# Kernel tuning notes

Measured on AMD Instinct MI355X. Metric: run time of the kernel, lower is better.

The kernel has to match this reference:

```python
import jax, jax.numpy as jnp
import numpy as np

NH, NKV, HD = 16, 8, 128  # heads, kv heads, head dim
N_REP = NH // NKV
EPS = 1e-06
K_MASK = float(jnp.finfo(jnp.bfloat16).min)
SCALE = HD ** -0.5


def _rms_norm(x, w):
    xf = x.astype(jnp.float32)
    rms = jnp.sqrt(jnp.mean(xf * xf, axis=-1, keepdims=True) + EPS)
    return (xf / rms * w).astype(x.dtype)


def _rotate_half(x):
    x1, x2 = jnp.split(x, 2, axis=-1)
    return jnp.concatenate([-x2, x1], axis=-1)


def setup_inputs() -> dict:
    key = jax.random.key(0)
    ks = jax.random.split(key, 5)
    B, S, H = 1, 2048, 2048
    hidden_states = jax.random.normal(ks[0], (B, S, H), jnp.float32)
    # real RoPE tables (duplicated-half layout), theta = 5e6
    pos = jnp.arange(S, dtype=jnp.float32)
    inv_freq = 1.0 / (5_000_000.0 ** (jnp.arange(0, HD, 2, dtype=jnp.float32) / HD))
    ang = pos[:, None] * inv_freq[None, :]            # (S, HD/2)
    emb = jnp.concatenate([ang, ang], axis=-1)[None]  # (1, S, HD)
    cos, sin = jnp.cos(emb), jnp.sin(emb)
    attention_mask = jnp.tril(jnp.ones((S, S), bool))[None, None]  # causal (1,1,S,S)
    sc = 0.02
    wq = jax.random.normal(ks[1], (H, NH * HD), jnp.float32) * sc
    wk = jax.random.normal(ks[2], (H, NKV * HD), jnp.float32) * sc
    wv = jax.random.normal(ks[3], (H, NKV * HD), jnp.float32) * sc
    wo = jax.random.normal(ks[4], (NH * HD, H), jnp.float32) * sc
    q_norm_w = jnp.ones((HD,), jnp.float32)
    k_norm_w = jnp.ones((HD,), jnp.float32)
    return {"hidden_states": hidden_states, "cos": cos, "sin": sin,
            "attention_mask": attention_mask, "wq": wq, "wk": wk, "wv": wv,
            "wo": wo, "q_norm_w": q_norm_w, "k_norm_w": k_norm_w}


def reference(hidden_states, cos, sin, attention_mask, wq, wk, wv, wo, q_norm_w, k_norm_w):
    B, S, H = hidden_states.shape
    q = (hidden_states @ wq).reshape(B, S, NH, HD)
    k = (hidden_states @ wk).reshape(B, S, NKV, HD)
    v = (hidden_states @ wv).reshape(B, S, NKV, HD)
    q = _rms_norm(q, q_norm_w)
    k = _rms_norm(k, k_norm_w)
    c = cos[:, :, None, :]
    s = sin[:, :, None, :]
    q = q * c + _rotate_half(q) * s
    k = k * c + _rotate_half(k) * s
    # GQA: group q heads by kv head; same math as jnp.repeat + matmul
    qg = q.reshape(B, S, NKV, N_REP, HD)
    scores = jnp.einsum('bqgrd,bkgd->bgrqk', qg, k) * SCALE  # (B,NKV,N_REP,S,S)
    scores = jnp.where(attention_mask[:, :, None], scores, K_MASK)
    attn = jax.nn.softmax(scores.astype(jnp.float32), axis=-1).astype(q.dtype)
    out = jnp.einsum('bgrqk,bkgd->bqgrd', attn, v)            # (B,S,NKV,N_REP,HD)
    out = out.reshape(B, S, NH * HD)
    return out @ wo
```

## Files before the change

kernel.cpp:

```cpp
#include <hip/hip_runtime.h>
#include <hip/hip_bf16.h>
#include <stdint.h>

typedef _Float16 half8 __attribute__((ext_vector_type(8)));
typedef _Float16 half4 __attribute__((ext_vector_type(4)));
typedef float f32x4 __attribute__((ext_vector_type(4)));

#define MFMA16(A, B, C) __builtin_amdgcn_mfma_f32_16x16x32_f16(A, B, C, 0, 0, 0)

static constexpr int Sdim = 2048;
static constexpr int NH = 16;
static constexpr int NKV = 8;
static constexpr int HD = 128;
static constexpr float ATT_SCALE = 0.08838834764831845f;
static constexpr float S0 = 4.0f;

__device__ __forceinline__ void async_copy16(const _Float16* g, _Float16* l) {
  auto gp = reinterpret_cast<const __attribute__((address_space(1))) uint32_t*>(
      reinterpret_cast<uintptr_t>(g));
  auto lp = reinterpret_cast<__attribute__((address_space(3))) uint32_t*>(
      reinterpret_cast<uintptr_t>(l));
  __builtin_amdgcn_global_load_lds(gp, lp, 16, 0, 0);
}

__global__ __launch_bounds__(256) void xconv(const float* __restrict__ X,
                                             _Float16* __restrict__ Xh) {
  int i = (blockIdx.x * 256 + threadIdx.x) * 4;
  float4 v = *(const float4*)(X + i);
  half4 h = {(_Float16)v.x, (_Float16)v.y, (_Float16)v.z, (_Float16)v.w};
  *(half4*)(Xh + i) = h;
}

__global__ __launch_bounds__(256) void wtrans_all(const float* __restrict__ wq,
                                                  const float* __restrict__ wk,
                                                  const float* __restrict__ wv,
                                                  const float* __restrict__ wo,
                                                  _Float16* __restrict__ wqT,
                                                  _Float16* __restrict__ wkT,
                                                  _Float16* __restrict__ wvT,
                                                  _Float16* __restrict__ woT) {
  const float* W;
  _Float16* WT;
  int N;
  switch (blockIdx.z) {
    case 0: W = wq; WT = wqT; N = 2048; break;
    case 1: W = wk; WT = wkT; N = 1024; break;
    case 2: W = wv; WT = wvT; N = 1024; break;
    default: W = wo; WT = woT; N = 2048; break;
  }
  if ((int)blockIdx.x * 64 >= N) return;
  const int K = 2048;
  __shared__ __align__(16) float tile[64][68];
  int n0 = blockIdx.x * 64, k0 = blockIdx.y * 64;
  int t = threadIdx.x;
  int c = (t & 15) * 4;
  int rb = t >> 4;
  for (int p = 0; p < 4; ++p) {
    int k = p * 16 + rb;
    *(float4*)&tile[k][c] = *(const float4*)(W + (size_t)(k0 + k) * N + n0 + c);
  }
  __syncthreads();
  int n = t >> 2;
  int kc = (t & 3) * 16;
  half8 o0, o1;
  for (int i = 0; i < 8; ++i) {
    o0[i] = (_Float16)tile[kc + i][n];
    o1[i] = (_Float16)tile[kc + 8 + i][n];
  }
  _Float16* dst = WT + (size_t)(n0 + n) * K + k0 + kc;
  *(half8*)dst = o0;
  *(half8*)(dst + 8) = o1;
}

template <int NI>
__device__ __forceinline__ void stage64(const _Float16* __restrict__ src, size_t stride,
                                        int k0, _Float16* lds, int w, int lane) {
  for (int ii = 0; ii < NI; ++ii) {
    int i = w * NI + ii;
    int row = i * 8 + (lane >> 3);
    int c = (lane & 7) ^ (row & 7);
    async_copy16(src + (size_t)row * stride + k0 + c * 8, lds + i * 512);
  }
}

__device__ __forceinline__ int frag_off(int row, int ks, int quad, int col) {
  return row * 64 + (((ks << 2) | quad) ^ (col & 7)) * 8;
}

__global__ __launch_bounds__(256) void gemm_qkv(const _Float16* __restrict__ Xh,
                                                const _Float16* __restrict__ wqT,
                                                const _Float16* __restrict__ wkT,
                                                const _Float16* __restrict__ wvT,
                                                _Float16* __restrict__ Q,
                                                _Float16* __restrict__ K,
                                                _Float16* __restrict__ Vt) {
  __shared__ __align__(16) _Float16 As[128 * 64];
  __shared__ __align__(16) _Float16 Bs[128 * 64];
  int bx = blockIdx.x, m0 = blockIdx.y * 128;
  const _Float16* BT;
  _Float16* outp;
  int n0, Nst;
  bool vt;
  if (bx < 16)      { BT = wqT; outp = Q;  n0 = bx * 128;        vt = false; Nst = 2048; }
  else if (bx < 24) { BT = wkT; outp = K;  n0 = (bx - 16) * 128; vt = false; Nst = 1024; }
  else              { BT = wvT; outp = Vt; n0 = (bx - 24) * 128; vt = true;  Nst = 2048; }
  int t = threadIdx.x, lane = t & 63, w = t >> 6;
  int col = lane & 15, quad = lane >> 4;
  int wm = (w & 1) * 64, wn = (w >> 1) * 64;
  f32x4 acc[4][4] = {};
  for (int k0 = 0; k0 < 2048; k0 += 64) {
    stage64<4>(Xh + (size_t)m0 * 2048, 2048, k0, As, w, lane);
    stage64<4>(BT + (size_t)n0 * 2048, 2048, k0, Bs, w, lane);
    __syncthreads();
    half8 af[4][2], bf[4][2];
    for (int i = 0; i < 4; ++i)
      for (int ks = 0; ks < 2; ++ks) {
        af[i][ks] = *(const half8*)(As + frag_off(wm + i * 16 + col, ks, quad, col));
        bf[i][ks] = *(const half8*)(Bs + frag_off(wn + i * 16 + col, ks, quad, col));
      }
    if (!vt) {
      for (int ks = 0; ks < 2; ++ks)
        for (int i = 0; i < 4; ++i)
          for (int j = 0; j < 4; ++j)
            acc[i][j] = MFMA16(bf[j][ks], af[i][ks], acc[i][j]);
    } else {
      for (int ks = 0; ks < 2; ++ks)
        for (int i = 0; i < 4; ++i)
          for (int j = 0; j < 4; ++j)
            acc[i][j] = MFMA16(af[i][ks], bf[j][ks], acc[i][j]);
    }
    __syncthreads();
  }
  if (!vt) {
    for (int i = 0; i < 4; ++i)
      for (int j = 0; j < 4; ++j) {
        int m = m0 + wm + i * 16 + col;
        int n = n0 + wn + j * 16 + quad * 4;
        half4 hv = {(_Float16)acc[i][j][0], (_Float16)acc[i][j][1],
                    (_Float16)acc[i][j][2], (_Float16)acc[i][j][3]};
        *(half4*)(outp + (size_t)m * Nst + n) = hv;
      }
  } else {
    for (int i = 0; i < 4; ++i)
      for (int j = 0; j < 4; ++j) {
        int n = n0 + wn + j * 16 + col;
        int mb = m0 + wm + i * 16 + quad * 4;
        half4 hv = {(_Float16)acc[i][j][0], (_Float16)acc[i][j][1],
                    (_Float16)acc[i][j][2], (_Float16)acc[i][j][3]};
        *(half4*)(outp + (size_t)n * Sdim + mb) = hv;
      }
  }
}

__global__ __launch_bounds__(256) void gemm_o(const _Float16* __restrict__ A,
                                              const _Float16* __restrict__ BT,
                                              float* __restrict__ C) {
  __shared__ __align__(16) _Float16 As[64 * 64];
  __shared__ __align__(16) _Float16 Bs[128 * 64];
  int m0 = blockIdx.y * 64, n0 = blockIdx.x * 128;
  int t = threadIdx.x, lane = t & 63, w = t >> 6;
  int col = lane & 15, quad = lane >> 4;
  int wm = (w & 1) * 32, wn = (w >> 1) * 64;
  f32x4 acc[2][4] = {};
  for (int k0 = 0; k0 < 2048; k0 += 64) {
    stage64<2>(A + (size_t)m0 * 2048, 2048, k0, As, w, lane);
    stage64<4>(BT + (size_t)n0 * 2048, 2048, k0, Bs, w, lane);
    __syncthreads();
    half8 af[2][2], bf[4][2];
    for (int ks = 0; ks < 2; ++ks) {
      for (int i = 0; i < 2; ++i)
        af[i][ks] = *(const half8*)(As + frag_off(wm + i * 16 + col, ks, quad, col));
      for (int j = 0; j < 4; ++j)
        bf[j][ks] = *(const half8*)(Bs + frag_off(wn + j * 16 + col, ks, quad, col));
    }
    for (int ks = 0; ks < 2; ++ks)
      for (int i = 0; i < 2; ++i)
        for (int j = 0; j < 4; ++j)
          acc[i][j] = MFMA16(bf[j][ks], af[i][ks], acc[i][j]);
    __syncthreads();
  }
  for (int i = 0; i < 2; ++i)
    for (int j = 0; j < 4; ++j) {
      int m = m0 + wm + i * 16 + col;
      int n = n0 + wn + j * 16 + quad * 4;
      *(f32x4*)(C + (size_t)m * 2048 + n) = acc[i][j];
    }
}

__global__ __launch_bounds__(256) void rmsrope_all(const _Float16* __restrict__ Qraw,
                                                   const _Float16* __restrict__ Kraw,
                                                   _Float16* __restrict__ Qn,
                                                   _Float16* __restrict__ Kn,
                                                   const float* __restrict__ cs,
                                                   const float* __restrict__ sn,
                                                   const float* __restrict__ qw,
                                                   const float* __restrict__ kw) {
  int w = threadIdx.x >> 6, lane = threadIdx.x & 63;
  int gw = blockIdx.x * 4 + w;
  const _Float16* src;
  _Float16* dst;
  const float* nw;
  int m, h, nh;
  float scale;
  if (gw < Sdim * NH) {
    m = gw >> 4; h = gw & 15; nh = NH; src = Qraw; dst = Qn; nw = qw; scale = ATT_SCALE;
  } else {
    int g2 = gw - Sdim * NH;
    m = g2 >> 3; h = g2 & 7; nh = NKV; src = Kraw; dst = Kn; nw = kw; scale = 1.0f;
  }
  const _Float16* p = src + (size_t)m * nh * HD + h * HD;
  float x0 = (float)p[lane], x1 = (float)p[lane + 64];
  float ss = x0 * x0 + x1 * x1;
#pragma unroll
  for (int o = 32; o > 0; o >>= 1) ss += __shfl_xor(ss, o);
  float inv = rsqrtf(ss * (1.0f / 128.0f) + 1e-6f);
  float n0v = x0 * inv * nw[lane], n1v = x1 * inv * nw[lane + 64];
  float c0 = cs[m * HD + lane], c1 = cs[m * HD + lane + 64];
  float s0 = sn[m * HD + lane], s1 = sn[m * HD + lane + 64];
  _Float16* q = dst + (size_t)m * nh * HD + h * HD;
  q[lane] = (_Float16)((n0v * c0 - n1v * s0) * scale);
  q[lane + 64] = (_Float16)((n1v * c1 + n0v * s1) * scale);
}

__device__ __forceinline__ void attn_tile(const half8* qf, f32x4* O, float* li,
                                          const _Float16* Ksb, const _Float16* Vsb,
                                          _Float16* Psw, bool domask,
                                          int col, int quad, int w) {
  f32x4 Sc[4];
  __builtin_amdgcn_s_setprio(1);
  for (int nt = 0; nt < 4; ++nt) {
    f32x4 a = {};
    for (int kc = 0; kc < 4; ++kc) {
      half8 b = *(const half8*)(Ksb + (nt * 16 + col) * 128 + ((4 * kc + quad) ^ col) * 8);
      a = MFMA16(qf[kc], b, a);
    }
    Sc[nt] = a;
  }
  __builtin_amdgcn_s_setprio(0);
  if (domask) {
    for (int nt = 0; nt < 4; ++nt)
      for (int r = 0; r < 4; ++r)
        if ((nt * 16 + col) > (w * 16 + quad * 4 + r)) Sc[nt][r] = -1e4f;
  }
  for (int nt = 0; nt < 4; ++nt)
    for (int r = 0; r < 4; ++r) {
      float pv = __expf(Sc[nt][r] - S0);
      Sc[nt][r] = pv;
      li[r] += pv;
    }
  for (int nt = 0; nt < 4; ++nt)
    for (int r = 0; r < 4; ++r) {
      int q = quad * 4 + r;
      Psw[q * 64 + (((2 * nt + (col >> 3)) ^ (q & 7)) * 8) + (col & 7)] =
          (_Float16)Sc[nt][r];
    }
  __builtin_amdgcn_s_setprio(1);
  for (int c2 = 0; c2 < 2; ++c2) {
    half8 ap = *(const half8*)(Psw + col * 64 + (((4 * c2 + quad) ^ (col & 7)) * 8));
    for (int nt = 0; nt < 8; ++nt) {
      half8 bv = *(const half8*)(Vsb + (nt * 16 + col) * 64 +
                                 (((4 * c2 + quad) ^ (col & 7)) * 8));
      O[nt] = MFMA16(ap, bv, O[nt]);
    }
  }
  __builtin_amdgcn_s_setprio(0);
}

__global__ __launch_bounds__(256, 2) void fattn(const _Float16* __restrict__ Qn,
                                                const _Float16* __restrict__ Kn,
                                                const _Float16* __restrict__ Vt,
                                                _Float16* __restrict__ Op01,
                                                float* __restrict__ lp) {
  __shared__ __align__(16) _Float16 Ks[2][64 * 128];
  __shared__ __align__(16) _Float16 Vs[2][128 * 64];
  __shared__ __align__(16) _Float16 Ps[4 * 1024];
  int f = blockIdx.x;
  int Wk = (f & 7) * 64 + (f >> 3);
  int xb = Wk & 15, h = (Wk >> 4) & 15, s = Wk >> 8;
  int g = h >> 1;
  int qb0 = 31 - xb, qb1 = xb;
  int t = threadIdx.x, lane = t & 63, w = t >> 6;
  int col = lane & 15, quad = lane >> 4;
  _Float16* Psw = Ps + w * 1024;
  _Float16* op = Op01 + (size_t)s * Sdim * (NH * HD);
  float* lpp = lp + (size_t)s * NH * Sdim + (size_t)h * Sdim;

  auto stageKV = [&](int b, int kt) {
    for (int ii = 0; ii < 4; ++ii) {
      int i = w * 4 + ii;
      int krow = i * 4 + (lane >> 4);
      int kc = (lane & 15) ^ (krow & 15);
      async_copy16(Kn + (size_t)(kt * 64 + krow) * (NKV * HD) + g * HD + kc * 8,
                   Ks[b] + i * 512);
      int vrow = i * 8 + (lane >> 3);
      int vc = (lane & 7) ^ (vrow & 7);
      async_copy16(Vt + (size_t)(g * HD + vrow) * Sdim + kt * 64 + vc * 8,
                   Vs[b] + i * 512);
    }
  };

  half8 qf0[4], qf1[4];
  {
    int qr0 = qb0 * 64 + w * 16 + col;
    int qr1 = qb1 * 64 + w * 16 + col;
    for (int kc = 0; kc < 4; ++kc) {
      qf0[kc] = *(const half8*)(Qn + (size_t)qr0 * (NH * HD) + h * HD + kc * 32 + quad * 8);
      qf1[kc] = *(const half8*)(Qn + (size_t)qr1 * (NH * HD) + h * HD + kc * 32 + quad * 8);
    }
  }
  f32x4 O0[8] = {}, O1[8] = {};
  float li0[4] = {}, li1[4] = {};

  int nt = (qb0 - s) / 2 + 1;
  stageKV(0, s);
#pragma unroll 1
  for (int it = 0; it < nt; ++it) {
    int kt = s + it * 2;
    int c = it & 1;
    if (it + 1 < nt) {
      stageKV(c ^ 1, kt + 2);
      asm volatile("s_waitcnt vmcnt(8)" ::: "memory");
    } else {
      asm volatile("s_waitcnt vmcnt(0)" ::: "memory");
    }
    __builtin_amdgcn_sched_barrier(0);
    __builtin_amdgcn_s_barrier();
    __builtin_amdgcn_sched_barrier(0);
    const _Float16* Kb = Ks[c];
    const _Float16* Vb = Vs[c];
    if (kt <= qb1) {
      attn_tile(qf0, O0, li0, Kb, Vb, Psw, false, col, quad, w);
      attn_tile(qf1, O1, li1, Kb, Vb, Psw, kt == qb1, col, quad, w);
    } else {
      attn_tile(qf0, O0, li0, Kb, Vb, Psw, kt == qb0, col, quad, w);
    }
    __builtin_amdgcn_sched_barrier(0);
    __builtin_amdgcn_s_barrier();
    __builtin_amdgcn_sched_barrier(0);
  }

  auto finish = [&](f32x4* O, float* li, int qb) {
    for (int r = 0; r < 4; ++r) {
      float sm = li[r];
      sm += __shfl_xor(sm, 1);
      sm += __shfl_xor(sm, 2);
      sm += __shfl_xor(sm, 4);
      sm += __shfl_xor(sm, 8);
      li[r] = sm;
    }
    for (int ntile = 0; ntile < 8; ++ntile)
      for (int r = 0; r < 4; ++r) {
        int m = qb * 64 + w * 16 + quad * 4 + r;
        op[(size_t)m * (NH * HD) + h * HD + ntile * 16 + col] = (_Float16)O[ntile][r];
      }
    if (col == 0)
      for (int r = 0; r < 4; ++r) lpp[qb * 64 + w * 16 + quad * 4 + r] = li[r];
  };
  finish(O0, li0, qb0);
  finish(O1, li1, qb1);
}

__global__ __launch_bounds__(256) void merge(const _Float16* __restrict__ Op01,
                                             const float* __restrict__ lp,
                                             _Float16* __restrict__ attn) {
  int m = blockIdx.x, t = threadIdx.x;
  int h = t >> 4, d0 = (t & 15) * 8;
  size_t off = (size_t)m * (NH * HD) + h * HD + d0;
  half8 o0 = *(const half8*)(Op01 + off);
  half8 o1 = *(const half8*)(Op01 + (size_t)Sdim * NH * HD + off);
  float l = lp[(size_t)h * Sdim + m] +
            lp[(size_t)NH * Sdim + (size_t)h * Sdim + m];
  float ri = 1.0f / l;
  half8 o;
  for (int i = 0; i < 8; ++i)
    o[i] = (_Float16)(((float)o0[i] + (float)o1[i]) * ri);
  *(half8*)(attn + off) = o;
}

extern "C" void kernel_launch(void* const* d_in, const int* in_sizes, int n_in,
                              void* d_out, int out_size, void* d_ws, size_t ws_size,
                              hipStream_t stream) {
  (void)in_sizes; (void)n_in; (void)out_size; (void)ws_size;
  const float* X  = (const float*)d_in[0];
  const float* cs = (const float*)d_in[1];
  const float* sn = (const float*)d_in[2];
  const float* wq = (const float*)d_in[4];
  const float* wk = (const float*)d_in[5];
  const float* wv = (const float*)d_in[6];
  const float* wo = (const float*)d_in[7];
  const float* qw = (const float*)d_in[8];
  const float* kw = (const float*)d_in[9];
  char* ws = (char*)d_ws;
  const size_t MB = 1024 * 1024;
  _Float16* wqT  = (_Float16*)(ws + 0 * MB);
  _Float16* wkT  = (_Float16*)(ws + 8 * MB);
  _Float16* wvT  = (_Float16*)(ws + 12 * MB);
  _Float16* woT  = (_Float16*)(ws + 16 * MB);
  _Float16* Xh   = (_Float16*)(ws + 24 * MB);
  _Float16* Qraw = (_Float16*)(ws + 32 * MB);
  _Float16* Kraw = (_Float16*)(ws + 40 * MB);
  _Float16* Vt   = (_Float16*)(ws + 44 * MB);
  _Float16* Qn   = (_Float16*)(ws + 48 * MB);
  _Float16* Kn   = (_Float16*)(ws + 56 * MB);
  float*    lp   = (float*)(ws + 60 * MB);
  _Float16* Op01 = wqT;
  _Float16* attn = Qraw;
  float* out = (float*)d_out;

  xconv<<<4096, 256, 0, stream>>>(X, Xh);
  wtrans_all<<<dim3(32, 32, 4), 256, 0, stream>>>(wq, wk, wv, wo, wqT, wkT, wvT, woT);

  gemm_qkv<<<dim3(32, 16), 256, 0, stream>>>(Xh, wqT, wkT, wvT, Qraw, Kraw, Vt);

  rmsrope_all<<<(Sdim * NH + Sdim * NKV) / 4, 256, 0, stream>>>(Qraw, Kraw, Qn, Kn,
                                                                cs, sn, qw, kw);

  fattn<<<512, 256, 0, stream>>>(Qn, Kn, Vt, Op01, lp);
  merge<<<2048, 256, 0, stream>>>(Op01, lp, attn);

  gemm_o<<<dim3(16, 32), 256, 0, stream>>>(attn, woT, out);
}
```

Measured before the change: 251.1 us.

## Double-buffer LDS in QKV and output GEMMs with async prefetch pipeline

Result: no change. 250.5 us (-0.2%).

```diff
diff --git a/kernel.cpp b/kernel.cpp
--- a/kernel.cpp
+++ b/kernel.cpp
@@ -87,15 +87,15 @@
   return row * 64 + (((ks << 2) | quad) ^ (col & 7)) * 8;
 }
 
-__global__ __launch_bounds__(256) void gemm_qkv(const _Float16* __restrict__ Xh,
-                                                const _Float16* __restrict__ wqT,
-                                                const _Float16* __restrict__ wkT,
-                                                const _Float16* __restrict__ wvT,
-                                                _Float16* __restrict__ Q,
-                                                _Float16* __restrict__ K,
-                                                _Float16* __restrict__ Vt) {
-  __shared__ __align__(16) _Float16 As[128 * 64];
-  __shared__ __align__(16) _Float16 Bs[128 * 64];
+__global__ __launch_bounds__(256, 2) void gemm_qkv(const _Float16* __restrict__ Xh,
+                                                   const _Float16* __restrict__ wqT,
+                                                   const _Float16* __restrict__ wkT,
+                                                   const _Float16* __restrict__ wvT,
+                                                   _Float16* __restrict__ Q,
+                                                   _Float16* __restrict__ K,
+                                                   _Float16* __restrict__ Vt) {
+  __shared__ __align__(16) _Float16 As[2][128 * 64];
+  __shared__ __align__(16) _Float16 Bs[2][128 * 64];
   int bx = blockIdx.x, m0 = blockIdx.y * 128;
   const _Float16* BT;
   _Float16* outp;
@@ -107,17 +107,31 @@
   int t = threadIdx.x, lane = t & 63, w = t >> 6;
   int col = lane & 15, quad = lane >> 4;
   int wm = (w & 1) * 64, wn = (w >> 1) * 64;
+  const _Float16* Ap = Xh + (size_t)m0 * 2048;
+  const _Float16* Bp = BT + (size_t)n0 * 2048;
   f32x4 acc[4][4] = {};
-  for (int k0 = 0; k0 < 2048; k0 += 64) {
-    stage64<4>(Xh + (size_t)m0 * 2048, 2048, k0, As, w, lane);
-    stage64<4>(BT + (size_t)n0 * 2048, 2048, k0, Bs, w, lane);
-    __syncthreads();
+  stage64<4>(Ap, 2048, 0, As[0], w, lane);
+  stage64<4>(Bp, 2048, 0, Bs[0], w, lane);
+#pragma unroll 1
+  for (int it = 0; it < 32; ++it) {
+    int c = it & 1;
+    if (it + 1 < 32) {
+      stage64<4>(Ap, 2048, (it + 1) * 64, As[c ^ 1], w, lane);
+      stage64<4>(Bp, 2048, (it + 1) * 64, Bs[c ^ 1], w, lane);
+      asm volatile("s_waitcnt vmcnt(8)" ::: "memory");
+    } else {
+      asm volatile("s_waitcnt vmcnt(0)" ::: "memory");
+    }
+    __builtin_amdgcn_sched_barrier(0);
+    __builtin_amdgcn_s_barrier();
+    __builtin_amdgcn_sched_barrier(0);
     half8 af[4][2], bf[4][2];
     for (int i = 0; i < 4; ++i)
       for (int ks = 0; ks < 2; ++ks) {
-        af[i][ks] = *(const half8*)(As + frag_off(wm + i * 16 + col, ks, quad, col));
-        bf[i][ks] = *(const half8*)(Bs + frag_off(wn + i * 16 + col, ks, quad, col));
+        af[i][ks] = *(const half8*)(As[c] + frag_off(wm + i * 16 + col, ks, quad, col));
+        bf[i][ks] = *(const half8*)(Bs[c] + frag_off(wn + i * 16 + col, ks, quad, col));
       }
+    __builtin_amdgcn_s_setprio(1);
     if (!vt) {
       for (int ks = 0; ks < 2; ++ks)
         for (int i = 0; i < 4; ++i)
@@ -129,7 +143,10 @@
           for (int j = 0; j < 4; ++j)
             acc[i][j] = MFMA16(af[i][ks], bf[j][ks], acc[i][j]);
     }
-    __syncthreads();
+    __builtin_amdgcn_s_setprio(0);
+    __builtin_amdgcn_sched_barrier(0);
+    __builtin_amdgcn_s_barrier();
+    __builtin_amdgcn_sched_barrier(0);
   }
   if (!vt) {
     for (int i = 0; i < 4; ++i)
@@ -152,32 +169,49 @@
   }
 }
 
-__global__ __launch_bounds__(256) void gemm_o(const _Float16* __restrict__ A,
-                                              const _Float16* __restrict__ BT,
-                                              float* __restrict__ C) {
-  __shared__ __align__(16) _Float16 As[64 * 64];
-  __shared__ __align__(16) _Float16 Bs[128 * 64];
+__global__ __launch_bounds__(256, 2) void gemm_o(const _Float16* __restrict__ A,
+                                                 const _Float16* __restrict__ BT,
+                                                 float* __restrict__ C) {
+  __shared__ __align__(16) _Float16 As[2][64 * 64];
+  __shared__ __align__(16) _Float16 Bs[2][128 * 64];
   int m0 = blockIdx.y * 64, n0 = blockIdx.x * 128;
   int t = threadIdx.x, lane = t & 63, w = t >> 6;
   int col = lane & 15, quad = lane >> 4;
   int wm = (w & 1) * 32, wn = (w >> 1) * 64;
+  const _Float16* Ap = A + (size_t)m0 * 2048;
+  const _Float16* Bp = BT + (size_t)n0 * 2048;
   f32x4 acc[2][4] = {};
-  for (int k0 = 0; k0 < 2048; k0 += 64) {
-    stage64<2>(A + (size_t)m0 * 2048, 2048, k0, As, w, lane);
-    stage64<4>(BT + (size_t)n0 * 2048, 2048, k0, Bs, w, lane);
-    __syncthreads();
+  stage64<2>(Ap, 2048, 0, As[0], w, lane);
+  stage64<4>(Bp, 2048, 0, Bs[0], w, lane);
+#pragma unroll 1
+  for (int it = 0; it < 32; ++it) {
+    int c = it & 1;
+    if (it + 1 < 32) {
+      stage64<2>(Ap, 2048, (it + 1) * 64, As[c ^ 1], w, lane);
+      stage64<4>(Bp, 2048, (it + 1) * 64, Bs[c ^ 1], w, lane);
+      asm volatile("s_waitcnt vmcnt(6)" ::: "memory");
+    } else {
+      asm volatile("s_waitcnt vmcnt(0)" ::: "memory");
+    }
+    __builtin_amdgcn_sched_barrier(0);
+    __builtin_amdgcn_s_barrier();
+    __builtin_amdgcn_sched_barrier(0);
     half8 af[2][2], bf[4][2];
     for (int ks = 0; ks < 2; ++ks) {
       for (int i = 0; i < 2; ++i)
-        af[i][ks] = *(const half8*)(As + frag_off(wm + i * 16 + col, ks, quad, col));
+        af[i][ks] = *(const half8*)(As[c] + frag_off(wm + i * 16 + col, ks, quad, col));
       for (int j = 0; j < 4; ++j)
-        bf[j][ks] = *(const half8*)(Bs + frag_off(wn + j * 16 + col, ks, quad, col));
-    }
+        bf[j][ks] = *(const half8*)(Bs[c] + frag_off(wn + j * 16 + col, ks, quad, col));
+    }
+    __builtin_amdgcn_s_setprio(1);
     for (int ks = 0; ks < 2; ++ks)
       for (int i = 0; i < 2; ++i)
         for (int j = 0; j < 4; ++j)
           acc[i][j] = MFMA16(bf[j][ks], af[i][ks], acc[i][j]);
-    __syncthreads();
+    __builtin_amdgcn_s_setprio(0);
+    __builtin_amdgcn_sched_barrier(0);
+    __builtin_amdgcn_s_barrier();
+    __builtin_amdgcn_sched_barrier(0);
   }
   for (int i = 0; i < 2; ++i)
     for (int j = 0; j < 4; ++j) {
```
